# Kernel tuning notes

Measured on AMD Instinct MI355X. Metric: run time of the kernel, lower is better.

The kernel has to match this reference:

```python
import jax, jax.numpy as jnp
import numpy as np

B, S, D, H, F = 2, 4096, 768, 12, 3072
DK = D // H
EPS = 1e-5


def _layernorm(x, alpha, gamma):
    # Faithful to the custom Layernormalization: torch.std (unbiased, ddof=1),
    # (x - mean) / (std + eps), scalar alpha/gamma.
    m = jnp.mean(x, axis=-1, keepdims=True)
    s = jnp.std(x, axis=-1, ddof=1, keepdims=True)
    return alpha * ((x - m) / (s + EPS)) + gamma


def setup_inputs() -> dict:
    key = jax.random.key(0)
    ks = jax.random.split(key, 12)
    sc = 0.02
    inp = {
        "x": jax.random.normal(ks[0], (B, S, D), jnp.float32),
        # attention projections, stored as [in, out]
        "wq": jax.random.normal(ks[1], (D, D), jnp.float32) * sc,
        "bq": jnp.zeros((D,), jnp.float32),
        "wk": jax.random.normal(ks[2], (D, D), jnp.float32) * sc,
        "bk": jnp.zeros((D,), jnp.float32),
        "wv": jax.random.normal(ks[3], (D, D), jnp.float32) * sc,
        "bv": jnp.zeros((D,), jnp.float32),
        "wo": jax.random.normal(ks[4], (D, D), jnp.float32) * sc,
        "bo": jnp.zeros((D,), jnp.float32),
        # feedforward
        "w1": jax.random.normal(ks[5], (D, F), jnp.float32) * sc,
        "b1": jnp.zeros((F,), jnp.float32),
        "w2": jax.random.normal(ks[6], (F, D), jnp.float32) * sc,
        "b2": jnp.zeros((D,), jnp.float32),
        # two residual LayerNorms, scalar params (alpha=1, gamma=0 at init)
        "a1": jnp.ones((1,), jnp.float32),
        "g1": jnp.zeros((1,), jnp.float32),
        "a2": jnp.ones((1,), jnp.float32),
        "g2": jnp.zeros((1,), jnp.float32),
    }
    return inp


def reference(x, wq, bq, wk, bk, wv, bv, wo, bo, w1, b1, w2, b2, a1, g1, a2, g2):
    # --- self attention sublayer ---
    q = (x @ wq + bq).reshape(B, S, H, DK).transpose(0, 2, 1, 3)  # [B,H,S,dk]
    k = (x @ wk + bk).reshape(B, S, H, DK).transpose(0, 2, 1, 3)
    v = (x @ wv + bv).reshape(B, S, H, DK).transpose(0, 2, 1, 3)
    scores = jnp.einsum("bhqd,bhkd->bhqk", q, k) / np.sqrt(DK).astype(np.float32)
    attn = jax.nn.softmax(scores, axis=-1)  # dropout is identity (p=0 / eval)
    ctx = jnp.einsum("bhqk,bhkd->bhqd", attn, v)  # [B,H,S,dk]
    ctx = ctx.transpose(0, 2, 1, 3).reshape(B, S, D)
    attn_out = ctx @ wo + bo
    x = _layernorm(x + attn_out, a1, g1)
    # --- feedforward sublayer ---
    ff = jax.nn.relu(x @ w1 + b1) @ w2 + b2
    x = _layernorm(x + ff, a2, g2)
    return x
```

## Files before the change

### kernel.cpp

```cpp
#include <hip/hip_runtime.h>
#include <hip/hip_bf16.h>
#include <cstdint>
#include <cstddef>

typedef unsigned short u16;
typedef __attribute__((ext_vector_type(8))) __bf16 bf16x8;
typedef __attribute__((ext_vector_type(4))) float f32x4;

#define AS1 __attribute__((address_space(1)))
#define AS3 __attribute__((address_space(3)))

__device__ __forceinline__ u16 f2bf(float f) {
    union { float f; uint32_t u; } v; v.f = f;
    uint32_t r = (v.u + 0x7FFFu + ((v.u >> 16) & 1u)) >> 16;
    return (u16)r;
}

__device__ __forceinline__ float bf2f(u16 b) {
    union { uint32_t u; float f; } v; v.u = ((uint32_t)b) << 16;
    return v.f;
}

__device__ __forceinline__ uint32_t pack_bf2(float lo, float hi) {
    __hip_bfloat162 p = __float22bfloat162_rn(float2{lo, hi});
    union { __hip_bfloat162 b; uint32_t u; } v; v.b = p;
    return v.u;
}

__device__ __forceinline__ f32x4 mfma16(bf16x8 a, bf16x8 b, f32x4 c) {
    return __builtin_amdgcn_mfma_f32_16x16x32_bf16(a, b, c, 0, 0, 0);
}

__device__ __forceinline__ void async16(const u16* g, u16* lds_uniform_base) {
    __builtin_amdgcn_global_load_lds((const AS1 void*)g, (AS3 void*)lds_uniform_base, 16, 0, 0);
}

__global__ __launch_bounds__(256)
void k_prep(const float* __restrict__ x, u16* __restrict__ xb,
            const float* __restrict__ wq, const float* __restrict__ wk,
            const float* __restrict__ wv, const float* __restrict__ wo,
            const float* __restrict__ w1, const float* __restrict__ w2,
            u16* __restrict__ wqkvt, u16* __restrict__ wot,
            u16* __restrict__ w1t, u16* __restrict__ w2t)
{
    int bx = blockIdx.x;
    if (bx < 6144) {
        int i = (bx * 256 + threadIdx.x) * 4;
        float4 f = *(const float4*)(x + i);
        xb[i + 0] = f2bf(f.x); xb[i + 1] = f2bf(f.y);
        xb[i + 2] = f2bf(f.z); xb[i + 3] = f2bf(f.w);
        return;
    }
    int t = bx - 6144;
    const float* in; u16* out; int R, C;
    if (t < 2304) {
        int m = t / 576; t -= m * 576;
        R = 768; C = 768;
        in = (m == 0) ? wq : (m == 1) ? wk : (m == 2) ? wv : wo;
        out = (m < 3) ? wqkvt + (size_t)m * 768 * 768 : wot;
    } else if (t < 4608) {
        t -= 2304; in = w1; out = w1t; R = 768; C = 3072;
    } else {
        t -= 4608; in = w2; out = w2t; R = 3072; C = 768;
    }
    int tilesX = C >> 5;
    int c0 = (t % tilesX) * 32, r0 = (t / tilesX) * 32;
    __shared__ float tile[32][33];
    int tx = threadIdx.x & 31, ty = threadIdx.x >> 5;
    #pragma unroll
    for (int i = ty; i < 32; i += 8)
        tile[i][tx] = in[(size_t)(r0 + i) * C + c0 + tx];
    __syncthreads();
    #pragma unroll
    for (int i = ty; i < 32; i += 8)
        out[(size_t)(c0 + i) * R + r0 + tx] = f2bf(tile[tx][i]);
}

template <bool RELU>
__global__ __launch_bounds__(256)
void k_gemm(const u16* __restrict__ A, const u16* __restrict__ Bt,
            const float* __restrict__ bias, u16* __restrict__ Cb,
            int M, int N, int K)
{
    __shared__ __align__(16) u16 lA[128 * 32];
    __shared__ __align__(16) u16 lB[128 * 32];
    const int tid = threadIdx.x;
    const int w = tid >> 6, lane = tid & 63;
    const int quad = lane >> 4, l15 = lane & 15;
    const int m0 = blockIdx.x * 128, n0 = blockIdx.y * 128;
    const int wm = (w >> 1) * 64, wn = (w & 1) * 64;
    const int sw = (quad ^ ((l15 >> 1) & 3)) * 8;

    const f32x4 fz = {0.f, 0.f, 0.f, 0.f};
    f32x4 acc[4][4];
    #pragma unroll
    for (int i = 0; i < 4; ++i)
        #pragma unroll
        for (int j = 0; j < 4; ++j) acc[i][j] = fz;

    for (int k0 = 0; k0 < K; k0 += 32) {
        #pragma unroll
        for (int r = 0; r < 2; ++r) {
            int c = r * 256 + tid;
            int row = c >> 2, ch = (c & 3) ^ ((row >> 1) & 3);
            async16(A + (size_t)(m0 + row) * K + k0 + ch * 8,
                    (u16*)lA + (size_t)(r * 256 + w * 64) * 8);
            async16(Bt + (size_t)(n0 + row) * K + k0 + ch * 8,
                    (u16*)lB + (size_t)(r * 256 + w * 64) * 8);
        }
        __syncthreads();
        bf16x8 af[4], bfr[4];
        #pragma unroll
        for (int i = 0; i < 4; ++i)
            af[i] = *(const bf16x8*)&lA[(wm + i * 16 + l15) * 32 + sw];
        #pragma unroll
        for (int j = 0; j < 4; ++j)
            bfr[j] = *(const bf16x8*)&lB[(wn + j * 16 + l15) * 32 + sw];
        #pragma unroll
        for (int i = 0; i < 4; ++i)
            #pragma unroll
            for (int j = 0; j < 4; ++j)
                acc[i][j] = mfma16(af[i], bfr[j], acc[i][j]);
        __syncthreads();
    }
    #pragma unroll
    for (int j = 0; j < 4; ++j) {
        int col = n0 + wn + j * 16 + l15;
        float bv = bias[col];
        #pragma unroll
        for (int i = 0; i < 4; ++i) {
            int row = m0 + wm + i * 16 + quad * 4;
            #pragma unroll
            for (int r = 0; r < 4; ++r) {
                float t = acc[i][j][r] + bv;
                if (RELU) t = fmaxf(t, 0.f);
                Cb[(size_t)(row + r) * N + col] = f2bf(t);
            }
        }
    }
}

__global__ __launch_bounds__(256)
void k_gemm_part(const u16* __restrict__ A, const u16* __restrict__ Bt,
                 float* __restrict__ C0, float* __restrict__ C1,
                 int M, int N, int K, int Kh)
{
    __shared__ __align__(16) u16 lA[128 * 32];
    __shared__ __align__(16) u16 lB[128 * 32];
    const int tid = threadIdx.x;
    const int w = tid >> 6, lane = tid & 63;
    const int quad = lane >> 4, l15 = lane & 15;
    const int m0 = blockIdx.x * 128, n0 = blockIdx.y * 128;
    const int wm = (w >> 1) * 64, wn = (w & 1) * 64;
    const int sw = (quad ^ ((l15 >> 1) & 3)) * 8;
    const int kbeg = blockIdx.z * Kh, kend = kbeg + Kh;
    float* __restrict__ C = blockIdx.z ? C1 : C0;

    const f32x4 fz = {0.f, 0.f, 0.f, 0.f};
    f32x4 acc[4][4];
    #pragma unroll
    for (int i = 0; i < 4; ++i)
        #pragma unroll
        for (int j = 0; j < 4; ++j) acc[i][j] = fz;

    for (int k0 = kbeg; k0 < kend; k0 += 32) {
        #pragma unroll
        for (int r = 0; r < 2; ++r) {
            int c = r * 256 + tid;
            int row = c >> 2, ch = (c & 3) ^ ((row >> 1) & 3);
            async16(A + (size_t)(m0 + row) * K + k0 + ch * 8,
                    (u16*)lA + (size_t)(r * 256 + w * 64) * 8);
            async16(Bt + (size_t)(n0 + row) * K + k0 + ch * 8,
                    (u16*)lB + (size_t)(r * 256 + w * 64) * 8);
        }
        __syncthreads();
        bf16x8 af[4], bfr[4];
        #pragma unroll
        for (int i = 0; i < 4; ++i)
            af[i] = *(const bf16x8*)&lA[(wm + i * 16 + l15) * 32 + sw];
        #pragma unroll
        for (int j = 0; j < 4; ++j)
            bfr[j] = *(const bf16x8*)&lB[(wn + j * 16 + l15) * 32 + sw];
        #pragma unroll
        for (int i = 0; i < 4; ++i)
            #pragma unroll
            for (int j = 0; j < 4; ++j)
                acc[i][j] = mfma16(af[i], bfr[j], acc[i][j]);
        __syncthreads();
    }
    #pragma unroll
    for (int j = 0; j < 4; ++j) {
        int col = n0 + wn + j * 16 + l15;
        #pragma unroll
        for (int i = 0; i < 4; ++i) {
            int row = m0 + wm + i * 16 + quad * 4;
            #pragma unroll
            for (int r = 0; r < 4; ++r)
                C[(size_t)(row + r) * N + col] = acc[i][j][r];
        }
    }
}

__global__ __launch_bounds__(256)
void k_gemm_qkv(const u16* __restrict__ A, const u16* __restrict__ Bt,
                const float* __restrict__ bq, const float* __restrict__ bk,
                const float* __restrict__ bv,
                u16* __restrict__ qb, u16* __restrict__ kb, u16* __restrict__ vtg,
                int M, int K, float scale_q)
{
    __shared__ __align__(16) u16 qsm[4 * 64 * 72];
    u16* lA = qsm;
    u16* lB = qsm + 4096;
    const int tid = threadIdx.x;
    const int w = tid >> 6, lane = tid & 63;
    const int quad = lane >> 4, l15 = lane & 15;
    const int m0 = blockIdx.x * 128, n0 = blockIdx.y * 128;
    const int wm = (w >> 1) * 64, wn = (w & 1) * 64;
    const int sw = (quad ^ ((l15 >> 1) & 3)) * 8;
    const int sel = blockIdx.y / 6;
    const int cl0 = n0 - sel * 768;

    const f32x4 fz = {0.f, 0.f, 0.f, 0.f};
    f32x4 acc[4][4];
    #pragma unroll
    for (int i = 0; i < 4; ++i)
        #pragma unroll
        for (int j = 0; j < 4; ++j) acc[i][j] = fz;

    for (int k0 = 0; k0 < K; k0 += 32) {
        #pragma unroll
        for (int r = 0; r < 2; ++r) {
            int c = r * 256 + tid;
            int row = c >> 2, ch = (c & 3) ^ ((row >> 1) & 3);
            async16(A + (size_t)(m0 + row) * K + k0 + ch * 8,
                    lA + (size_t)(r * 256 + w * 64) * 8);
            async16(Bt + (size_t)(n0 + row) * K + k0 + ch * 8,
                    lB + (size_t)(r * 256 + w * 64) * 8);
        }
        __syncthreads();
        bf16x8 af[4], bfr[4];
        #pragma unroll
        for (int i = 0; i < 4; ++i)
            af[i] = *(const bf16x8*)&lA[(wm + i * 16 + l15) * 32 + sw];
        #pragma unroll
        for (int j = 0; j < 4; ++j)
            bfr[j] = *(const bf16x8*)&lB[(wn + j * 16 + l15) * 32 + sw];
        #pragma unroll
        for (int i = 0; i < 4; ++i)
            #pragma unroll
            for (int j = 0; j < 4; ++j)
                acc[i][j] = mfma16(af[i], bfr[j], acc[i][j]);
        __syncthreads();
    }
    const float* bias = (sel == 0) ? bq : (sel == 1) ? bk : bv;
    if (sel < 2) {
        u16* out = (sel == 0) ? qb : kb;
        float sc = (sel == 0) ? scale_q : 1.f;
        #pragma unroll
        for (int j = 0; j < 4; ++j) {
            int cl = cl0 + wn + j * 16 + l15;
            float bvv = bias[cl];
            #pragma unroll
            for (int i = 0; i < 4; ++i) {
                int row = m0 + wm + i * 16 + quad * 4;
                #pragma unroll
                for (int r = 0; r < 4; ++r)
                    out[(size_t)(row + r) * 768 + cl] = f2bf((acc[i][j][r] + bvv) * sc);
            }
        }
    } else {
        u16* lT = qsm + w * 4608;
        #pragma unroll
        for (int j = 0; j < 4; ++j) {
            float bvv = bias[cl0 + wn + j * 16 + l15];
            #pragma unroll
            for (int i = 0; i < 4; ++i)
                #pragma unroll
                for (int r = 0; r < 4; ++r)
                    lT[(j * 16 + l15) * 72 + i * 16 + quad * 4 + r]
                        = f2bf(acc[i][j][r] + bvv);
        }
        int gcol = cl0 + wn + lane;
        u16* gdst = vtg + (size_t)gcol * M + m0 + wm;
        #pragma unroll
        for (int kk = 0; kk < 8; ++kk) {
            bf16x8 v = *(const bf16x8*)&lT[lane * 72 + kk * 8];
            *(bf16x8*)(gdst + kk * 8) = v;
        }
    }
}

__global__ __launch_bounds__(256, 3)
void k_attention(const u16* __restrict__ Q, const u16* __restrict__ Kb,
                 const u16* __restrict__ Vt, u16* __restrict__ ctx,
                 int S, int D, int H, int M)
{
    __shared__ __align__(16) u16 sKV[16384];
    __shared__ float sL[2][64];
    const int qt = blockIdx.x, bh = blockIdx.y;
    const int b = bh / H, h = bh % H;
    const int tid = threadIdx.x, w = tid >> 6, lane = tid & 63;
    const int wq = w & 1, wk = w >> 1;
    const int quad = lane >> 4, l15 = lane & 15;
    const int sw = (quad ^ ((l15 >> 1) & 3)) * 8;
    const size_t bS = (size_t)b * S;
    const int q0 = qt * 128 + wq * 64;

    bf16x8 qf[4][2];
    #pragma unroll
    for (int set = 0; set < 4; ++set)
        #pragma unroll
        for (int kc = 0; kc < 2; ++kc)
            qf[set][kc] = *(const bf16x8*)(Q + (bS + q0 + set * 16 + l15) * D
                                           + (size_t)h * 64 + kc * 32 + quad * 8);

    const f32x4 fz = {0.f, 0.f, 0.f, 0.f};
    f32x4 O[4][4];
    #pragma unroll
    for (int s = 0; s < 4; ++s)
        #pragma unroll
        for (int j = 0; j < 4; ++j) O[s][j] = fz;
    float l_[4] = {0.f, 0.f, 0.f, 0.f};

    const u16* kbase = Kb + bS * D + (size_t)h * 64;
    const u16* vbase = Vt + (size_t)h * 64 * M + bS;

    const u16* gk[2]; const u16* gv[2];
    #pragma unroll
    for (int i = 0; i < 2; ++i) {
        int c = i * 256 + tid;
        int kc = c >> 8;
        int krow = (c >> 2) & 63, kch = (c & 3) ^ ((krow >> 1) & 3);
        gk[i] = kbase + (size_t)krow * D + kc * 32 + kch * 8;
        int dk = (c >> 2) & 63, vch = (c & 3) ^ ((dk >> 1) & 3);
        gv[i] = vbase + (size_t)dk * M + kc * 32 + vch * 8;
    }
    const int dslot = (w * 64) * 8;

    #pragma unroll
    for (int i = 0; i < 2; ++i) {
        async16(gk[i], sKV + i * 2048 + dslot);
        async16(gv[i], sKV + 8192 + i * 2048 + dslot);
        gk[i] += (size_t)64 * D;
        gv[i] += 64;
    }

    int rrow[2], swk[2];
    #pragma unroll
    for (int ks = 0; ks < 2; ++ks) {
        rrow[ks] = (l15 >> 2) * 8 + ks * 4 + (l15 & 3);
        swk[ks] = (quad ^ ((rrow[ks] >> 1) & 3)) * 8;
    }

    const int T = S >> 6;
    for (int t = 0; t < T; ++t) {
        __syncthreads();
        if (t + 1 < T) {
            int nb = (t + 1) & 1;
            #pragma unroll
            for (int i = 0; i < 2; ++i) {
                async16(gk[i], sKV + nb * 4096 + i * 2048 + dslot);
                async16(gv[i], sKV + 8192 + nb * 4096 + i * 2048 + dslot);
                gk[i] += (size_t)64 * D;
                gv[i] += 64;
            }
        }
        const u16* lKb = sKV + (t & 1) * 4096;
        const u16* lVb = sKV + 8192 + (t & 1) * 4096;

        bf16x8 ka[2][2], vf[4];
        #pragma unroll
        for (int ks = 0; ks < 2; ++ks)
            #pragma unroll
            for (int kc = 0; kc < 2; ++kc)
                ka[ks][kc] = *(const bf16x8*)
                    &lKb[kc * 2048 + (wk * 32 + rrow[ks]) * 32 + swk[ks]];
        #pragma unroll
        for (int dj = 0; dj < 4; ++dj)
            vf[dj] = *(const bf16x8*)
                &lVb[wk * 2048 + (dj * 16 + l15) * 32 + sw];

        #pragma unroll
        for (int set = 0; set < 4; ++set) {
            f32x4 sc0 = fz, sc1 = fz;
            __builtin_amdgcn_s_setprio(1);
            sc0 = mfma16(ka[0][0], qf[set][0], sc0);
            sc0 = mfma16(ka[0][1], qf[set][1], sc0);
            sc1 = mfma16(ka[1][0], qf[set][0], sc1);
            sc1 = mfma16(ka[1][1], qf[set][1], sc1);
            __builtin_amdgcn_s_setprio(0);
            float p0[4], p1[4];
            float rs = 0.f;
            #pragma unroll
            for (int r = 0; r < 4; ++r) {
                p0[r] = __builtin_amdgcn_exp2f(sc0[r]);
                p1[r] = __builtin_amdgcn_exp2f(sc1[r]);
                rs += p0[r] + p1[r];
            }
            l_[set] += rs;
            union { uint32_t u[4]; bf16x8 v; } pa;
            pa.u[0] = pack_bf2(p0[0], p0[1]); pa.u[1] = pack_bf2(p0[2], p0[3]);
            pa.u[2] = pack_bf2(p1[0], p1[1]); pa.u[3] = pack_bf2(p1[2], p1[3]);
            __builtin_amdgcn_s_setprio(1);
            #pragma unroll
            for (int dj = 0; dj < 4; ++dj)
                O[set][dj] = mfma16(pa.v, vf[dj], O[set][dj]);
            __builtin_amdgcn_s_setprio(0);
        }
    }

    float lred[4];
    #pragma unroll
    for (int set = 0; set < 4; ++set) {
        float lt = l_[set];
        lt += __shfl_xor(lt, 16, 64);
        lt += __shfl_xor(lt, 32, 64);
        lred[set] = lt;
    }
    __syncthreads();
    u16* lO = sKV;
    if (wk == 1) {
        #pragma unroll
        for (int set = 0; set < 4; ++set) {
            #pragma unroll
            for (int dj = 0; dj < 4; ++dj)
                #pragma unroll
                for (int r = 0; r < 4; ++r)
                    lO[(wq * 64 + set * 16 + quad * 4 + r) * 66 + dj * 16 + l15]
                        = f2bf(O[set][dj][r]);
            if (lane < 16) sL[wq][set * 16 + lane] = lred[set];
        }
    }
    __syncthreads();
    if (wk == 0) {
        #pragma unroll
        for (int set = 0; set < 4; ++set) {
            float ltot = lred[set] + sL[wq][set * 16 + l15];
            float rl[4];
            #pragma unroll
            for (int r = 0; r < 4; ++r)
                rl[r] = 1.f / __shfl(ltot, quad * 4 + r, 64);
            #pragma unroll
            for (int dj = 0; dj < 4; ++dj)
                #pragma unroll
                for (int r = 0; r < 4; ++r) {
                    float o = O[set][dj][r]
                        + bf2f(lO[(wq * 64 + set * 16 + quad * 4 + r) * 66 + dj * 16 + l15]);
                    ctx[(bS + q0 + set * 16 + quad * 4 + r) * D
                        + (size_t)h * 64 + dj * 16 + l15] = f2bf(o * rl[r]);
                }
        }
    }
}

__global__ __launch_bounds__(256)
void k_layernorm2(const float* __restrict__ p0, const float* __restrict__ p1,
                  const float* __restrict__ resid, const float* __restrict__ bias,
                  const float* __restrict__ a, const float* __restrict__ g,
                  float* __restrict__ outf, u16* __restrict__ outb, int D)
{
    const int row = blockIdx.x, tid = threadIdx.x;
    const size_t base = (size_t)row * D;
    float v[3];
    float s = 0.f, sq = 0.f;
    #pragma unroll
    for (int i = 0; i < 3; ++i) {
        int c = tid + i * 256;
        float x = p0[base + c] + p1[base + c] + resid[base + c] + bias[c];
        v[i] = x; s += x; sq += x * x;
    }
    #pragma unroll
    for (int off = 32; off >= 1; off >>= 1) {
        s += __shfl_xor(s, off, 64);
        sq += __shfl_xor(sq, off, 64);
    }
    __shared__ float red[8];
    const int w = tid >> 6;
    if ((tid & 63) == 0) { red[w] = s; red[4 + w] = sq; }
    __syncthreads();
    s = red[0] + red[1] + red[2] + red[3];
    sq = red[4] + red[5] + red[6] + red[7];
    float mean = s / D;
    float var = fmaxf((sq - s * mean) / (D - 1), 0.f);
    float denom = sqrtf(var) + 1e-5f;
    float av = a[0], gv = g[0];
    #pragma unroll
    for (int i = 0; i < 3; ++i) {
        float y = av * ((v[i] - mean) / denom) + gv;
        if (outf) outf[base + tid + i * 256] = y;
        if (outb) outb[base + tid + i * 256] = f2bf(y);
    }
}

extern "C" void kernel_launch(void* const* d_in, const int* in_sizes, int n_in,
                              void* d_out, int out_size, void* d_ws, size_t ws_size,
                              hipStream_t stream)
{
    constexpr int B = 2, S = 4096, D = 768, H = 12, F = 3072;
    constexpr int M = B * S;
    const float SCALE_Q = 1.4426950408889634f / 8.0f;
    const float* x  = (const float*)d_in[0];
    const float* wq = (const float*)d_in[1];
    const float* bq = (const float*)d_in[2];
    const float* wk = (const float*)d_in[3];
    const float* bk = (const float*)d_in[4];
    const float* wv = (const float*)d_in[5];
    const float* bv = (const float*)d_in[6];
    const float* wo = (const float*)d_in[7];
    const float* bo = (const float*)d_in[8];
    const float* w1 = (const float*)d_in[9];
    const float* b1 = (const float*)d_in[10];
    const float* w2 = (const float*)d_in[11];
    const float* b2 = (const float*)d_in[12];
    const float* a1 = (const float*)d_in[13];
    const float* g1 = (const float*)d_in[14];
    const float* a2 = (const float*)d_in[15];
    const float* g2 = (const float*)d_in[16];

    char* ws = (char*)d_ws;
    size_t off = 0;
    auto alloc = [&](size_t bytes) {
        void* p = ws + off;
        off = (off + bytes + 255) & ~(size_t)255;
        return p;
    };
    u16*   xb    = (u16*)alloc((size_t)M * D * 2);
    u16*   wqkvt = (u16*)alloc((size_t)3 * D * D * 2);
    u16*   wot   = (u16*)alloc((size_t)D * D * 2);
    u16*   w1t   = (u16*)alloc((size_t)D * F * 2);
    u16*   w2t   = (u16*)alloc((size_t)D * F * 2);
    u16*   qb    = (u16*)alloc((size_t)M * D * 2);
    u16*   kb    = (u16*)alloc((size_t)M * D * 2);
    u16*   vtg   = (u16*)alloc((size_t)M * D * 2);
    u16*   ctxb  = (u16*)alloc((size_t)M * D * 2);
    float* x1f   = (float*)alloc((size_t)M * D * 4);
    u16*   x1b   = (u16*)alloc((size_t)M * D * 2);
    u16*   ff1b  = (u16*)alloc((size_t)M * F * 2);

    float* p0a = (float*)qb;
    float* p1a = (float*)ff1b;
    float* p0b = (float*)qb;
    float* p1b = (float*)vtg;

    k_prep<<<6144 + 6912, 256, 0, stream>>>(x, xb, wq, wk, wv, wo, w1, w2,
                                            wqkvt, wot, w1t, w2t);

    k_gemm_qkv<<<dim3(M / 128, 3 * D / 128), 256, 0, stream>>>(
        xb, wqkvt, bq, bk, bv, qb, kb, vtg, M, D, SCALE_Q);

    k_attention<<<dim3(S / 128, B * H), 256, 0, stream>>>(qb, kb, vtg, ctxb, S, D, H, M);

    k_gemm_part<<<dim3(M / 128, D / 128, 2), 256, 0, stream>>>(
        ctxb, wot, p0a, p1a, M, D, D, D / 2);
    k_layernorm2<<<M, 256, 0, stream>>>(p0a, p1a, x, bo, a1, g1, x1f, x1b, D);

    k_gemm<true><<<dim3(M / 128, F / 128), 256, 0, stream>>>(
        x1b, w1t, b1, ff1b, M, F, D);
    k_gemm_part<<<dim3(M / 128, D / 128, 2), 256, 0, stream>>>(
        ff1b, w2t, p0b, p1b, M, D, F, F / 2);
    k_layernorm2<<<M, 256, 0, stream>>>(p0b, p1b, x1f, b2, a2, g2, (float*)d_out, nullptr, D);

    (void)in_sizes; (void)n_in; (void)out_size; (void)ws_size;
}
```

Before: 482.5 us.

## Split attention KV range across two blocks and add a combine kernel

The attention kernel gains a grid z-dimension of 2, so each block handles half of the key/value sequence. Each block writes unnormalized fp32 partial outputs and row sums, and a new combine kernel adds the two halves, normalizes and writes the bf16 context. The K-tile shared-memory swizzle also gets an extra XOR term to cut bank conflicts. The split doubles the number of blocks, at the cost of a large fp32 partial write and read plus an extra kernel launch; the partials buffer reuses the ff1b workspace.

```diff
diff --git a/kernel.cpp b/kernel.cpp
--- a/kernel.cpp
+++ b/kernel.cpp
@@ -292,12 +292,13 @@
 
 __global__ __launch_bounds__(256, 3)
 void k_attention(const u16* __restrict__ Q, const u16* __restrict__ Kb,
-                 const u16* __restrict__ Vt, u16* __restrict__ ctx,
+                 const u16* __restrict__ Vt, float* __restrict__ Opart,
+                 float* __restrict__ lpart,
                  int S, int D, int H, int M)
 {
     __shared__ __align__(16) u16 sKV[16384];
     __shared__ float sL[2][64];
-    const int qt = blockIdx.x, bh = blockIdx.y;
+    const int qt = blockIdx.x, bh = blockIdx.y, z = blockIdx.z;
     const int b = bh / H, h = bh % H;
     const int tid = threadIdx.x, w = tid >> 6, lane = tid & 63;
     const int wq = w & 1, wk = w >> 1;
@@ -305,6 +306,8 @@
     const int sw = (quad ^ ((l15 >> 1) & 3)) * 8;
     const size_t bS = (size_t)b * S;
     const int q0 = qt * 128 + wq * 64;
+    const size_t MD = (size_t)M * D, MH = (size_t)M * H;
+    const int halfS = S >> 1;
 
     bf16x8 qf[4][2];
     #pragma unroll
@@ -322,15 +325,16 @@
         for (int j = 0; j < 4; ++j) O[s][j] = fz;
     float l_[4] = {0.f, 0.f, 0.f, 0.f};
 
-    const u16* kbase = Kb + bS * D + (size_t)h * 64;
-    const u16* vbase = Vt + (size_t)h * 64 * M + bS;
+    const u16* kbase = Kb + (bS + z * halfS) * D + (size_t)h * 64;
+    const u16* vbase = Vt + (size_t)h * 64 * M + bS + z * halfS;
 
     const u16* gk[2]; const u16* gv[2];
     #pragma unroll
     for (int i = 0; i < 2; ++i) {
         int c = i * 256 + tid;
         int kc = c >> 8;
-        int krow = (c >> 2) & 63, kch = (c & 3) ^ ((krow >> 1) & 3);
+        int krow = (c >> 2) & 63;
+        int kch = (c & 3) ^ ((krow >> 1) & 3) ^ ((krow >> 3) & 3);
         gk[i] = kbase + (size_t)krow * D + kc * 32 + kch * 8;
         int dk = (c >> 2) & 63, vch = (c & 3) ^ ((dk >> 1) & 3);
         gv[i] = vbase + (size_t)dk * M + kc * 32 + vch * 8;
@@ -348,11 +352,13 @@
     int rrow[2], swk[2];
     #pragma unroll
     for (int ks = 0; ks < 2; ++ks) {
-        rrow[ks] = (l15 >> 2) * 8 + ks * 4 + (l15 & 3);
-        swk[ks] = (quad ^ ((rrow[ks] >> 1) & 3)) * 8;
-    }
-
-    const int T = S >> 6;
+        int rr = (l15 >> 2) * 8 + ks * 4 + (l15 & 3);
+        int row64 = wk * 32 + rr;
+        rrow[ks] = rr;
+        swk[ks] = (quad ^ ((row64 >> 1) & 3) ^ ((row64 >> 3) & 3)) * 8;
+    }
+
+    const int T = halfS >> 6;
     for (int t = 0; t < T; ++t) {
         __syncthreads();
         if (t + 1 < T) {
@@ -433,23 +439,39 @@
     }
     __syncthreads();
     if (wk == 0) {
+        float* Op = Opart + (size_t)z * MD;
+        float* lp = lpart + (size_t)z * MH;
         #pragma unroll
         for (int set = 0; set < 4; ++set) {
             float ltot = lred[set] + sL[wq][set * 16 + l15];
-            float rl[4];
-            #pragma unroll
-            for (int r = 0; r < 4; ++r)
-                rl[r] = 1.f / __shfl(ltot, quad * 4 + r, 64);
+            if (lane < 16)
+                lp[(bS + q0 + set * 16 + lane) * H + h] = ltot;
             #pragma unroll
             for (int dj = 0; dj < 4; ++dj)
                 #pragma unroll
                 for (int r = 0; r < 4; ++r) {
                     float o = O[set][dj][r]
                         + bf2f(lO[(wq * 64 + set * 16 + quad * 4 + r) * 66 + dj * 16 + l15]);
-                    ctx[(bS + q0 + set * 16 + quad * 4 + r) * D
-                        + (size_t)h * 64 + dj * 16 + l15] = f2bf(o * rl[r]);
+                    Op[(bS + q0 + set * 16 + quad * 4 + r) * D
+                       + (size_t)h * 64 + dj * 16 + l15] = o;
                 }
         }
+    }
+}
+
+__global__ __launch_bounds__(256)
+void k_attn_combine(const float* __restrict__ Opart, const float* __restrict__ lpart,
+                    u16* __restrict__ ctx, int D, int H, size_t MD, size_t MH)
+{
+    const int row = blockIdx.x, tid = threadIdx.x;
+    const size_t base = (size_t)row * D;
+    #pragma unroll
+    for (int i = 0; i < 3; ++i) {
+        int c = tid + i * 256;
+        int h = c >> 6;
+        float lt = lpart[(size_t)row * H + h] + lpart[MH + (size_t)row * H + h];
+        float o = Opart[base + c] + Opart[MD + base + c];
+        ctx[base + c] = f2bf(o / lt);
     }
 }
 
@@ -536,6 +558,9 @@
     float* x1f   = (float*)alloc((size_t)M * D * 4);
     u16*   x1b   = (u16*)alloc((size_t)M * D * 2);
     u16*   ff1b  = (u16*)alloc((size_t)M * F * 2);
+    float* lpart = (float*)alloc((size_t)2 * M * H * 4);
+
+    float* Opart = (float*)ff1b;
 
     float* p0a = (float*)qb;
     float* p1a = (float*)ff1b;
@@ -548,7 +573,10 @@
     k_gemm_qkv<<<dim3(M / 128, 3 * D / 128), 256, 0, stream>>>(
         xb, wqkvt, bq, bk, bv, qb, kb, vtg, M, D, SCALE_Q);
 
-    k_attention<<<dim3(S / 128, B * H), 256, 0, stream>>>(qb, kb, vtg, ctxb, S, D, H, M);
+    k_attention<<<dim3(S / 128, B * H, 2), 256, 0, stream>>>(
+        qb, kb, vtg, Opart, lpart, S, D, H, M);
+    k_attn_combine<<<M, 256, 0, stream>>>(
+        Opart, lpart, ctxb, D, H, (size_t)M * D, (size_t)M * H);
 
     k_gemm_part<<<dim3(M / 128, D / 128, 2), 256, 0, stream>>>(
         ctxb, wot, p0a, p1a, M, D, D, D / 2);
```

After: 494.1 us. +2.4%, slower.

## Compute softmax row sums via MFMA with ones vector and re-swizzle K LDS layout

Applied to the files above, without the earlier changes.

The softmax denominator was accumulated with scalar adds and cross-lane shuffles. It is now computed by an extra MFMA that multiplies the packed probabilities by a bf16 ones vector, so the row sums come out in the output-accumulator layout. The K tile's global-to-LDS load mapping and the LDS read addressing are also reorganised with a new row swizzle. The change trades VALU adds and shuffles for one more MFMA per set. The sum now comes from bf16-rounded probabilities, which matches the numerator more closely.

```diff
diff --git a/kernel.cpp b/kernel.cpp
--- a/kernel.cpp
+++ b/kernel.cpp
@@ -315,27 +315,30 @@
                                            + (size_t)h * 64 + kc * 32 + quad * 8);
 
     const f32x4 fz = {0.f, 0.f, 0.f, 0.f};
-    f32x4 O[4][4];
-    #pragma unroll
-    for (int s = 0; s < 4; ++s)
+    f32x4 O[4][4], Ol[4];
+    #pragma unroll
+    for (int s = 0; s < 4; ++s) {
+        Ol[s] = fz;
         #pragma unroll
         for (int j = 0; j < 4; ++j) O[s][j] = fz;
-    float l_[4] = {0.f, 0.f, 0.f, 0.f};
+    }
+    union { u16 s[8]; bf16x8 v; } one8;
+    #pragma unroll
+    for (int i = 0; i < 8; ++i) one8.s[i] = 0x3F80;
 
     const u16* kbase = Kb + bS * D + (size_t)h * 64;
     const u16* vbase = Vt + (size_t)h * 64 * M + bS;
 
+    const int rsw = (lane & ~12) | ((lane & 4) << 1) | ((lane & 8) >> 1);
     const u16* gk[2]; const u16* gv[2];
     #pragma unroll
     for (int i = 0; i < 2; ++i) {
+        gk[i] = kbase + (size_t)rsw * D + i * 32 + w * 8;
         int c = i * 256 + tid;
-        int kc = c >> 8;
-        int krow = (c >> 2) & 63, kch = (c & 3) ^ ((krow >> 1) & 3);
-        gk[i] = kbase + (size_t)krow * D + kc * 32 + kch * 8;
         int dk = (c >> 2) & 63, vch = (c & 3) ^ ((dk >> 1) & 3);
-        gv[i] = vbase + (size_t)dk * M + kc * 32 + vch * 8;
-    }
-    const int dslot = (w * 64) * 8;
+        gv[i] = vbase + (size_t)dk * M + i * 32 + vch * 8;
+    }
+    const int dslot = w * 512;
 
     #pragma unroll
     for (int i = 0; i < 2; ++i) {
@@ -345,11 +348,12 @@
         gv[i] += 64;
     }
 
-    int rrow[2], swk[2];
+    int ksl[2];
     #pragma unroll
     for (int ks = 0; ks < 2; ++ks) {
-        rrow[ks] = (l15 >> 2) * 8 + ks * 4 + (l15 & 3);
-        swk[ks] = (quad ^ ((rrow[ks] >> 1) & 3)) * 8;
+        int row64 = wk * 32 + ((l15 >> 2) << 3) + ks * 4 + (l15 & 3);
+        int s = (row64 & ~12) | ((row64 & 4) << 1) | ((row64 & 8) >> 1);
+        ksl[ks] = quad * 512 + s * 8;
     }
 
     const int T = S >> 6;
@@ -373,8 +377,7 @@
         for (int ks = 0; ks < 2; ++ks)
             #pragma unroll
             for (int kc = 0; kc < 2; ++kc)
-                ka[ks][kc] = *(const bf16x8*)
-                    &lKb[kc * 2048 + (wk * 32 + rrow[ks]) * 32 + swk[ks]];
+                ka[ks][kc] = *(const bf16x8*)&lKb[kc * 2048 + ksl[ks]];
         #pragma unroll
         for (int dj = 0; dj < 4; ++dj)
             vf[dj] = *(const bf16x8*)
@@ -390,14 +393,11 @@
             sc1 = mfma16(ka[1][1], qf[set][1], sc1);
             __builtin_amdgcn_s_setprio(0);
             float p0[4], p1[4];
-            float rs = 0.f;
             #pragma unroll
             for (int r = 0; r < 4; ++r) {
                 p0[r] = __builtin_amdgcn_exp2f(sc0[r]);
                 p1[r] = __builtin_amdgcn_exp2f(sc1[r]);
-                rs += p0[r] + p1[r];
             }
-            l_[set] += rs;
             union { uint32_t u[4]; bf16x8 v; } pa;
             pa.u[0] = pack_bf2(p0[0], p0[1]); pa.u[1] = pack_bf2(p0[2], p0[3]);
             pa.u[2] = pack_bf2(p1[0], p1[1]); pa.u[3] = pack_bf2(p1[2], p1[3]);
@@ -405,18 +405,11 @@
             #pragma unroll
             for (int dj = 0; dj < 4; ++dj)
                 O[set][dj] = mfma16(pa.v, vf[dj], O[set][dj]);
+            Ol[set] = mfma16(pa.v, one8.v, Ol[set]);
             __builtin_amdgcn_s_setprio(0);
         }
     }
 
-    float lred[4];
-    #pragma unroll
-    for (int set = 0; set < 4; ++set) {
-        float lt = l_[set];
-        lt += __shfl_xor(lt, 16, 64);
-        lt += __shfl_xor(lt, 32, 64);
-        lred[set] = lt;
-    }
     __syncthreads();
     u16* lO = sKV;
     if (wk == 1) {
@@ -428,18 +421,21 @@
                 for (int r = 0; r < 4; ++r)
                     lO[(wq * 64 + set * 16 + quad * 4 + r) * 66 + dj * 16 + l15]
                         = f2bf(O[set][dj][r]);
-            if (lane < 16) sL[wq][set * 16 + lane] = lred[set];
+            if (l15 == 0) {
+                #pragma unroll
+                for (int r = 0; r < 4; ++r)
+                    sL[wq][set * 16 + quad * 4 + r] = Ol[set][r];
+            }
         }
     }
     __syncthreads();
     if (wk == 0) {
         #pragma unroll
         for (int set = 0; set < 4; ++set) {
-            float ltot = lred[set] + sL[wq][set * 16 + l15];
             float rl[4];
             #pragma unroll
             for (int r = 0; r < 4; ++r)
-                rl[r] = 1.f / __shfl(ltot, quad * 4 + r, 64);
+                rl[r] = 1.f / (Ol[set][r] + sL[wq][set * 16 + quad * 4 + r]);
             #pragma unroll
             for (int dj = 0; dj < 4; ++dj)
                 #pragma unroll
```

Measured after the change: 473.3 us. No clear change (-1.9%).
